# Kernel tuning notes

Hardware: AMD Instinct MI355X
Metric: run time of the kernel (lower is better)

Reference implementation:

```python
import jax, jax.numpy as jnp
import numpy as np

N = 8192
FIN = 128
FOUT = 64
NEG_BIG = -9e15


def setup_inputs() -> dict:
    key = jax.random.key(0)
    k1, k2, k3, k4 = jax.random.split(key, 4)
    x = jax.random.normal(k1, (N, FIN), dtype=jnp.float32)
    adj = jax.random.randint(k2, (N, N), 0, 2, dtype=jnp.int32)
    stdv_w = 1.0 / np.sqrt(FOUT)
    W = jax.random.uniform(k3, (FIN, FOUT), dtype=jnp.float32, minval=-stdv_w, maxval=stdv_w)
    # weight2: stdv = 1/sqrt(1) = 1
    a = jax.random.uniform(k4, (2 * FOUT, 1), dtype=jnp.float32, minval=-1.0, maxval=1.0)
    return {"x": x, "adj": adj, "W": W, "a": a}


def reference(x, adj, W, a):
    # h = x W  -> [N, Fout]
    h = x @ W
    # e_ij = relu(a^T [h_i || h_j]) decomposed exactly: a1.h_i + a2.h_j
    a1 = a[:FOUT, 0]  # [Fout]
    a2 = a[FOUT:, 0]  # [Fout]
    s1 = h @ a1  # [N]
    s2 = h @ a2  # [N]
    e = jax.nn.relu(s1[:, None] + s2[None, :])  # [N, N]
    att_logits = jnp.where(adj > 0, e, jnp.float32(NEG_BIG))
    attention = jax.nn.softmax(att_logits, axis=-1)  # [N, N]
    # dropout omitted (eval mode / p applied only in training)
    out = attention @ h  # [N, Fout]
    return out[None]  # [1, N, Fout] matching batch_size=1 reshape
```

## Files before the change

### kernel.cpp

```cpp
#include <hip/hip_runtime.h>
#include <cstdint>
#include <cstddef>

#define NN 8192
#define FIN 128
#define FOUT 64
#define BM 32
#define BN 64
#define JSPLIT 8
#define JCH (NN / JSPLIT)
#define NCHUNK (JCH / BN)
#define LDP 72

typedef __bf16 bf16x8 __attribute__((ext_vector_type(8)));
typedef unsigned short u16x8 __attribute__((ext_vector_type(8)));
typedef float f32x4 __attribute__((ext_vector_type(4)));

__device__ __forceinline__ unsigned short f2bf(float f) {
    unsigned u = __float_as_uint(f);
    u += 0x7FFFu + ((u >> 16) & 1u);
    return (unsigned short)(u >> 16);
}
__device__ __forceinline__ float bf2f(unsigned short b) {
    return __uint_as_float(((unsigned)b) << 16);
}

__global__ __launch_bounds__(256) void gat_prep(
    const float* __restrict__ x, const float* __restrict__ W,
    const float* __restrict__ a, float* __restrict__ s1,
    float* __restrict__ s2, unsigned short* __restrict__ Ht,
    unsigned int* __restrict__ s2max_enc)
{
    __shared__ __align__(16) float Wt[FOUT][FIN + 4];
    __shared__ float wa1[FIN], wa2[FIN];
    __shared__ float ash[2 * FOUT];
    __shared__ float s2sh[BM];

    const int tid = threadIdx.x;
    const int i0 = blockIdx.x * BM;

    for (int it = 0; it < 32; ++it) {
        int idx = it * 256 + tid;
        int k = idx >> 6, t = idx & 63;
        Wt[t][k] = W[idx];
    }
    if (tid < 2 * FOUT) ash[tid] = a[tid];
    __syncthreads();

    if (tid < FIN) {
        int k = tid;
        float acc = 0.f;
        #pragma unroll 8
        for (int t = 0; t < FOUT; ++t) acc = fmaf(Wt[t][k], ash[t], acc);
        wa1[k] = acc;
    } else {
        int k = tid - FIN;
        float acc = 0.f;
        #pragma unroll 8
        for (int t = 0; t < FOUT; ++t) acc = fmaf(Wt[t][k], ash[FOUT + t], acc);
        wa2[k] = acc;
    }
    __syncthreads();

    {
        int r = tid >> 3;
        int seg = tid & 7;
        const float* xp = x + (size_t)(i0 + r) * FIN + seg * 16;
        float d1 = 0.f, d2 = 0.f;
        #pragma unroll
        for (int m = 0; m < 16; ++m) {
            float xv = xp[m];
            d1 = fmaf(xv, wa1[seg * 16 + m], d1);
            d2 = fmaf(xv, wa2[seg * 16 + m], d2);
        }
        #pragma unroll
        for (int mk = 1; mk < 8; mk <<= 1) {
            d1 += __shfl_xor(d1, mk);
            d2 += __shfl_xor(d2, mk);
        }
        if (seg == 0) {
            s1[i0 + r] = d1;
            s2[i0 + r] = d2;
            s2sh[r] = d2;
        }
    }

    {
        const int lane = tid & 63;
        const int wv = tid >> 6;
        const int ih = wv & 1, nh = wv >> 1;
        const int m = lane & 15, quad = lane >> 4;
        f32x4 hacc0 = {0.f, 0.f, 0.f, 0.f};
        f32x4 hacc1 = {0.f, 0.f, 0.f, 0.f};
        const float* xrow = x + (size_t)(i0 + ih * 16 + m) * FIN + quad * 8;
        #pragma unroll
        for (int ks = 0; ks < 4; ++ks) {
            const float* xp = xrow + ks * 32;
            u16x8 ua;
            #pragma unroll
            for (int jj = 0; jj < 8; ++jj) ua[jj] = f2bf(xp[jj]);
            bf16x8 af = __builtin_bit_cast(bf16x8, ua);
            {
                const float* wp = &Wt[nh * 32 + m][ks * 32 + quad * 8];
                u16x8 ub;
                #pragma unroll
                for (int jj = 0; jj < 8; ++jj) ub[jj] = f2bf(wp[jj]);
                bf16x8 bfr = __builtin_bit_cast(bf16x8, ub);
                hacc0 = __builtin_amdgcn_mfma_f32_16x16x32_bf16(af, bfr, hacc0, 0, 0, 0);
            }
            {
                const float* wp = &Wt[nh * 32 + 16 + m][ks * 32 + quad * 8];
                u16x8 ub;
                #pragma unroll
                for (int jj = 0; jj < 8; ++jj) ub[jj] = f2bf(wp[jj]);
                bf16x8 bfr = __builtin_bit_cast(bf16x8, ub);
                hacc1 = __builtin_amdgcn_mfma_f32_16x16x32_bf16(af, bfr, hacc1, 0, 0, 0);
            }
        }
        #pragma unroll
        for (int reg = 0; reg < 4; ++reg) {
            int irow = i0 + ih * 16 + quad * 4 + reg;
            int t0 = nh * 32 + m;
            Ht[(size_t)t0 * NN + irow] = f2bf(hacc0[reg]);
            Ht[(size_t)(t0 + 16) * NN + irow] = f2bf(hacc1[reg]);
        }
    }
    __syncthreads();
    if (tid == 0) {
        float mx = s2sh[0];
        #pragma unroll
        for (int r = 1; r < BM; ++r) mx = fmaxf(mx, s2sh[r]);
        unsigned ub = __float_as_uint(mx);
        unsigned enc = (ub & 0x80000000u) ? ~ub : (ub | 0x80000000u);
        atomicMax(s2max_enc, enc);
    }
}

__global__ __launch_bounds__(256, 6) void gat_attn(
    const int* __restrict__ adj, const float* __restrict__ s1,
    const float* __restrict__ s2, const unsigned short* __restrict__ Ht,
    const unsigned int* __restrict__ s2max_enc,
    float* __restrict__ pacc, float* __restrict__ pl)
{
    __shared__ __align__(16) unsigned short p_lds[2][BM][LDP];
    __shared__ __align__(16) float s2sh[JCH];
    __shared__ float s1v[BM], Mv[BM];

    const int tid = threadIdx.x;
    const int bx = blockIdx.x;
    const int r = bx >> 3;
    const int js = bx & 7;
    const int i0 = r * BM;
    const int j0 = js * JCH;

    const int li = tid >> 4;
    const int jg = (tid & 15) * 4;

    const int* adjp0 = adj + (size_t)(i0 + li) * NN + j0 + jg;
    const int* adjp1 = adjp0 + 16 * NN;

    int4 ca0 = *(const int4*)adjp0;
    int4 ca1 = *(const int4*)adjp1;

    const int lane = tid & 63;
    const int wv = tid >> 6;
    const int ih = wv & 1, nh = wv >> 1;
    const int cm = lane & 15, quad = lane >> 4;

    const unsigned short* htb0 = Ht + (size_t)(nh * 32 + cm) * NN + j0 + quad * 8;
    const unsigned short* htb1 = htb0 + (size_t)16 * NN;

    {
        int idx = tid * 4;
        *(float4*)&s2sh[idx] = *(const float4*)(s2 + j0 + idx);
        unsigned u = *s2max_enc;
        float S2MAX = (u & 0x80000000u) ? __uint_as_float(u ^ 0x80000000u)
                                        : __uint_as_float(~u);
        if (tid < BM) {
            float s = s1[i0 + tid];
            s1v[tid] = s;
            Mv[tid] = fmaxf(0.f, s + S2MAX);
        }
    }
    __syncthreads();

    f32x4 acc0 = {0.f, 0.f, 0.f, 0.f};
    f32x4 acc1 = {0.f, 0.f, 0.f, 0.f};
    float psA = 0.f, psB = 0.f;

    const float s1a = s1v[li], Ma = Mv[li];
    const float s1b = s1v[li + 16], Mb = Mv[li + 16];

    for (int c = 0; c < NCHUNK; ++c) {
        const int buf = c & 1;

        bf16x8 b00 = *(const bf16x8*)(htb0 + c * BN);
        bf16x8 b01 = *(const bf16x8*)(htb1 + c * BN);
        bf16x8 b10 = *(const bf16x8*)(htb0 + c * BN + 32);
        bf16x8 b11 = *(const bf16x8*)(htb1 + c * BN + 32);

        const int cn = (c + 1 < NCHUNK) ? (c + 1) : c;
        int4 na0 = *(const int4*)(adjp0 + cn * BN);
        int4 na1 = *(const int4*)(adjp1 + cn * BN);

        {
            const int* av0 = (const int*)&ca0;
            const int* av1 = (const int*)&ca1;
            const float* s2v = &s2sh[c * BN + jg];
            unsigned short qa[4], qb[4];
            #pragma unroll
            for (int jj = 0; jj < 4; ++jj) {
                float s2x = s2v[jj];
                float eA = fmaxf(s1a + s2x, 0.f);
                float pA = (av0[jj] > 0) ? __expf(eA - Ma) : 0.f;
                qa[jj] = f2bf(pA);
                psA += bf2f(qa[jj]);
                float eB = fmaxf(s1b + s2x, 0.f);
                float pB = (av1[jj] > 0) ? __expf(eB - Mb) : 0.f;
                qb[jj] = f2bf(pB);
                psB += bf2f(qb[jj]);
            }
            *(ushort4*)&p_lds[buf][li][jg]      = make_ushort4(qa[0], qa[1], qa[2], qa[3]);
            *(ushort4*)&p_lds[buf][li + 16][jg] = make_ushort4(qb[0], qb[1], qb[2], qb[3]);
        }

        __syncthreads();

        {
            bf16x8 af0 = *(const bf16x8*)&p_lds[buf][ih * 16 + cm][quad * 8];
            bf16x8 af1 = *(const bf16x8*)&p_lds[buf][ih * 16 + cm][32 + quad * 8];
            acc0 = __builtin_amdgcn_mfma_f32_16x16x32_bf16(af0, b00, acc0, 0, 0, 0);
            acc1 = __builtin_amdgcn_mfma_f32_16x16x32_bf16(af0, b01, acc1, 0, 0, 0);
            acc0 = __builtin_amdgcn_mfma_f32_16x16x32_bf16(af1, b10, acc0, 0, 0, 0);
            acc1 = __builtin_amdgcn_mfma_f32_16x16x32_bf16(af1, b11, acc1, 0, 0, 0);
        }

        ca0 = na0; ca1 = na1;
    }

    #pragma unroll
    for (int mk = 1; mk < 16; mk <<= 1) {
        psA += __shfl_xor(psA, mk);
        psB += __shfl_xor(psB, mk);
    }
    if ((tid & 15) == 0) {
        pl[(size_t)js * NN + i0 + li]      = psA;
        pl[(size_t)js * NN + i0 + li + 16] = psB;
    }

    #pragma unroll
    for (int reg = 0; reg < 4; ++reg) {
        int irow = i0 + ih * 16 + quad * 4 + reg;
        int n0 = nh * 32 + cm;
        pacc[((size_t)js * NN + irow) * FOUT + n0]      = acc0[reg];
        pacc[((size_t)js * NN + irow) * FOUT + n0 + 16] = acc1[reg];
    }
}

__global__ __launch_bounds__(256) void gat_combine(
    const float* __restrict__ pacc, const float* __restrict__ pl,
    float* __restrict__ out)
{
    int idx = blockIdx.x * 256 + threadIdx.x;
    int i = idx >> 6;
    float s = 0.f, l = 0.f;
    #pragma unroll
    for (int js = 0; js < JSPLIT; ++js) {
        s += pacc[(size_t)js * NN * FOUT + idx];
        l += pl[(size_t)js * NN + i];
    }
    out[idx] = s / l;
}

extern "C" void kernel_launch(void* const* d_in, const int* in_sizes, int n_in,
                              void* d_out, int out_size, void* d_ws, size_t ws_size,
                              hipStream_t stream) {
    const float* x   = (const float*)d_in[0];
    const int*   adj = (const int*)d_in[1];
    const float* W   = (const float*)d_in[2];
    const float* a   = (const float*)d_in[3];
    float* out = (float*)d_out;

    char* ws = (char*)d_ws;
    float* s1             = (float*)(ws);
    float* s2             = (float*)(ws + 32768);
    unsigned int* s2enc   = (unsigned int*)(ws + 65536);
    unsigned short* Ht    = (unsigned short*)(ws + 66560);
    float* pacc           = (float*)(ws + 66560 + 1048576);
    float* pl             = (float*)(ws + 66560 + 1048576 + 16777216);

    hipMemsetAsync(s2enc, 0, 4, stream);
    gat_prep<<<NN / BM, 256, 0, stream>>>(x, W, a, s1, s2, Ht, s2enc);
    gat_attn<<<(NN / BM) * JSPLIT, 256, 0, stream>>>(adj, s1, s2, Ht, s2enc, pacc, pl);
    gat_combine<<<NN * FOUT / 256, 256, 0, stream>>>(pacc, pl, out);
}
```

Measured before the change: 401.0 us.

## Compute P directly in MFMA A-operand registers, drop LDS staging and barriers

Each lane now builds its own attention-probability fragment in the layout the bf16 MFMA A operand expects. This removes the shared-memory P buffer and the per-chunk __syncthreads. Each wave now owns 16 rows and all 64 output columns (four accumulators), so the block tile grows to 64 rows and the grid halves. The intent is to remove LDS traffic and barrier stalls in this adj-bandwidth-bound loop. The cost is more Ht loads per wave, higher register pressure, and lower occupancy (launch bound 4).

```diff
diff --git a/kernel.cpp b/kernel.cpp
--- a/kernel.cpp
+++ b/kernel.cpp
@@ -6,11 +6,10 @@
 #define FIN 128
 #define FOUT 64
 #define BM 32
-#define BN 64
+#define AM 64
 #define JSPLIT 8
 #define JCH (NN / JSPLIT)
-#define NCHUNK (JCH / BN)
-#define LDP 72
+#define NCHUNK (JCH / 64)
 
 typedef __bf16 bf16x8 __attribute__((ext_vector_type(8)));
 typedef unsigned short u16x8 __attribute__((ext_vector_type(8)));
@@ -136,124 +135,118 @@
     }
 }
 
-__global__ __launch_bounds__(256, 6) void gat_attn(
+__device__ __forceinline__ void make_p(const int4 A, const int4 B,
+                                       const float* __restrict__ s2p,
+                                       float s1r, float M,
+                                       u16x8& ua, float& ps)
+{
+    const int av[8] = {A.x, A.y, A.z, A.w, B.x, B.y, B.z, B.w};
+    #pragma unroll
+    for (int jj = 0; jj < 8; ++jj) {
+        float e = fmaxf(s1r + s2p[jj], 0.f);
+        float pv = (av[jj] > 0) ? __expf(e - M) : 0.f;
+        unsigned short qv = f2bf(pv);
+        ua[jj] = qv;
+        ps += bf2f(qv);
+    }
+}
+
+__global__ __launch_bounds__(256, 4) void gat_attn(
     const int* __restrict__ adj, const float* __restrict__ s1,
     const float* __restrict__ s2, const unsigned short* __restrict__ Ht,
     const unsigned int* __restrict__ s2max_enc,
     float* __restrict__ pacc, float* __restrict__ pl)
 {
-    __shared__ __align__(16) unsigned short p_lds[2][BM][LDP];
     __shared__ __align__(16) float s2sh[JCH];
-    __shared__ float s1v[BM], Mv[BM];
 
     const int tid = threadIdx.x;
     const int bx = blockIdx.x;
     const int r = bx >> 3;
     const int js = bx & 7;
-    const int i0 = r * BM;
+    const int i0 = r * AM;
     const int j0 = js * JCH;
 
-    const int li = tid >> 4;
-    const int jg = (tid & 15) * 4;
-
-    const int* adjp0 = adj + (size_t)(i0 + li) * NN + j0 + jg;
-    const int* adjp1 = adjp0 + 16 * NN;
-
-    int4 ca0 = *(const int4*)adjp0;
-    int4 ca1 = *(const int4*)adjp1;
-
     const int lane = tid & 63;
-    const int wv = tid >> 6;
-    const int ih = wv & 1, nh = wv >> 1;
-    const int cm = lane & 15, quad = lane >> 4;
-
-    const unsigned short* htb0 = Ht + (size_t)(nh * 32 + cm) * NN + j0 + quad * 8;
-    const unsigned short* htb1 = htb0 + (size_t)16 * NN;
+    const int w = tid >> 6;
+    const int m = lane & 15;
+    const int q = lane >> 4;
+
+    const int irow = i0 + w * 16 + m;
 
     {
         int idx = tid * 4;
         *(float4*)&s2sh[idx] = *(const float4*)(s2 + j0 + idx);
-        unsigned u = *s2max_enc;
-        float S2MAX = (u & 0x80000000u) ? __uint_as_float(u ^ 0x80000000u)
-                                        : __uint_as_float(~u);
-        if (tid < BM) {
-            float s = s1[i0 + tid];
-            s1v[tid] = s;
-            Mv[tid] = fmaxf(0.f, s + S2MAX);
-        }
-    }
-    __syncthreads();
+    }
+    unsigned u = *s2max_enc;
+    const float S2MAX = (u & 0x80000000u) ? __uint_as_float(u ^ 0x80000000u)
+                                          : __uint_as_float(~u);
+    const float s1r = s1[irow];
+    const float M = fmaxf(0.f, s1r + S2MAX);
+    __syncthreads();
+
+    const int* adjr = adj + (size_t)irow * NN + j0 + q * 8;
+    const unsigned short* htb = Ht + (size_t)m * NN + j0 + q * 8;
 
     f32x4 acc0 = {0.f, 0.f, 0.f, 0.f};
     f32x4 acc1 = {0.f, 0.f, 0.f, 0.f};
-    float psA = 0.f, psB = 0.f;
-
-    const float s1a = s1v[li], Ma = Mv[li];
-    const float s1b = s1v[li + 16], Mb = Mv[li + 16];
+    f32x4 acc2 = {0.f, 0.f, 0.f, 0.f};
+    f32x4 acc3 = {0.f, 0.f, 0.f, 0.f};
+    float ps = 0.f;
+
+    int4 c0a = *(const int4*)(adjr);
+    int4 c0b = *(const int4*)(adjr + 4);
+    int4 c1a = *(const int4*)(adjr + 32);
+    int4 c1b = *(const int4*)(adjr + 36);
 
     for (int c = 0; c < NCHUNK; ++c) {
-        const int buf = c & 1;
-
-        bf16x8 b00 = *(const bf16x8*)(htb0 + c * BN);
-        bf16x8 b01 = *(const bf16x8*)(htb1 + c * BN);
-        bf16x8 b10 = *(const bf16x8*)(htb0 + c * BN + 32);
-        bf16x8 b11 = *(const bf16x8*)(htb1 + c * BN + 32);
-
-        const int cn = (c + 1 < NCHUNK) ? (c + 1) : c;
-        int4 na0 = *(const int4*)(adjp0 + cn * BN);
-        int4 na1 = *(const int4*)(adjp1 + cn * BN);
-
-        {
-            const int* av0 = (const int*)&ca0;
-            const int* av1 = (const int*)&ca1;
-            const float* s2v = &s2sh[c * BN + jg];
-            unsigned short qa[4], qb[4];
-            #pragma unroll
-            for (int jj = 0; jj < 4; ++jj) {
-                float s2x = s2v[jj];
-                float eA = fmaxf(s1a + s2x, 0.f);
-                float pA = (av0[jj] > 0) ? __expf(eA - Ma) : 0.f;
-                qa[jj] = f2bf(pA);
-                psA += bf2f(qa[jj]);
-                float eB = fmaxf(s1b + s2x, 0.f);
-                float pB = (av1[jj] > 0) ? __expf(eB - Mb) : 0.f;
-                qb[jj] = f2bf(pB);
-                psB += bf2f(qb[jj]);
-            }
-            *(ushort4*)&p_lds[buf][li][jg]      = make_ushort4(qa[0], qa[1], qa[2], qa[3]);
-            *(ushort4*)&p_lds[buf][li + 16][jg] = make_ushort4(qb[0], qb[1], qb[2], qb[3]);
-        }
-
-        __syncthreads();
-
-        {
-            bf16x8 af0 = *(const bf16x8*)&p_lds[buf][ih * 16 + cm][quad * 8];
-            bf16x8 af1 = *(const bf16x8*)&p_lds[buf][ih * 16 + cm][32 + quad * 8];
-            acc0 = __builtin_amdgcn_mfma_f32_16x16x32_bf16(af0, b00, acc0, 0, 0, 0);
-            acc1 = __builtin_amdgcn_mfma_f32_16x16x32_bf16(af0, b01, acc1, 0, 0, 0);
-            acc0 = __builtin_amdgcn_mfma_f32_16x16x32_bf16(af1, b10, acc0, 0, 0, 0);
-            acc1 = __builtin_amdgcn_mfma_f32_16x16x32_bf16(af1, b11, acc1, 0, 0, 0);
-        }
-
-        ca0 = na0; ca1 = na1;
-    }
-
-    #pragma unroll
-    for (int mk = 1; mk < 16; mk <<= 1) {
-        psA += __shfl_xor(psA, mk);
-        psB += __shfl_xor(psB, mk);
-    }
-    if ((tid & 15) == 0) {
-        pl[(size_t)js * NN + i0 + li]      = psA;
-        pl[(size_t)js * NN + i0 + li + 16] = psB;
-    }
-
+        const int cn = (c + 1 < NCHUNK) ? c + 1 : c;
+        const int* an = adjr + cn * 64;
+        int4 n0a = *(const int4*)(an);
+        int4 n0b = *(const int4*)(an + 4);
+        int4 n1a = *(const int4*)(an + 32);
+        int4 n1b = *(const int4*)(an + 36);
+
+        const unsigned short* hb = htb + c * 64;
+        bf16x8 b00 = *(const bf16x8*)(hb);
+        bf16x8 b01 = *(const bf16x8*)(hb + 32);
+        bf16x8 b10 = *(const bf16x8*)(hb + (size_t)16 * NN);
+        bf16x8 b11 = *(const bf16x8*)(hb + (size_t)16 * NN + 32);
+        bf16x8 b20 = *(const bf16x8*)(hb + (size_t)32 * NN);
+        bf16x8 b21 = *(const bf16x8*)(hb + (size_t)32 * NN + 32);
+        bf16x8 b30 = *(const bf16x8*)(hb + (size_t)48 * NN);
+        bf16x8 b31 = *(const bf16x8*)(hb + (size_t)48 * NN + 32);
+
+        const float* s2p = &s2sh[c * 64 + q * 8];
+        u16x8 ua0, ua1;
+        make_p(c0a, c0b, s2p,      s1r, M, ua0, ps);
+        make_p(c1a, c1b, s2p + 32, s1r, M, ua1, ps);
+        bf16x8 af0 = __builtin_bit_cast(bf16x8, ua0);
+        bf16x8 af1 = __builtin_bit_cast(bf16x8, ua1);
+
+        acc0 = __builtin_amdgcn_mfma_f32_16x16x32_bf16(af0, b00, acc0, 0, 0, 0);
+        acc1 = __builtin_amdgcn_mfma_f32_16x16x32_bf16(af0, b10, acc1, 0, 0, 0);
+        acc2 = __builtin_amdgcn_mfma_f32_16x16x32_bf16(af0, b20, acc2, 0, 0, 0);
+        acc3 = __builtin_amdgcn_mfma_f32_16x16x32_bf16(af0, b30, acc3, 0, 0, 0);
+        acc0 = __builtin_amdgcn_mfma_f32_16x16x32_bf16(af1, b01, acc0, 0, 0, 0);
+        acc1 = __builtin_amdgcn_mfma_f32_16x16x32_bf16(af1, b11, acc1, 0, 0, 0);
+        acc2 = __builtin_amdgcn_mfma_f32_16x16x32_bf16(af1, b21, acc2, 0, 0, 0);
+        acc3 = __builtin_amdgcn_mfma_f32_16x16x32_bf16(af1, b31, acc3, 0, 0, 0);
+
+        c0a = n0a; c0b = n0b; c1a = n1a; c1b = n1b;
+    }
+
+    ps += __shfl_xor(ps, 16);
+    ps += __shfl_xor(ps, 32);
+    if (q == 0) pl[(size_t)js * NN + irow] = ps;
+
+    const int orow = i0 + w * 16 + q * 4;
+    float* pb = pacc + ((size_t)js * NN + orow) * FOUT + m;
     #pragma unroll
     for (int reg = 0; reg < 4; ++reg) {
-        int irow = i0 + ih * 16 + quad * 4 + reg;
-        int n0 = nh * 32 + cm;
-        pacc[((size_t)js * NN + irow) * FOUT + n0]      = acc0[reg];
-        pacc[((size_t)js * NN + irow) * FOUT + n0 + 16] = acc1[reg];
+        pb[(size_t)reg * FOUT]      = acc0[reg];
+        pb[(size_t)reg * FOUT + 16] = acc1[reg];
+        pb[(size_t)reg * FOUT + 32] = acc2[reg];
+        pb[(size_t)reg * FOUT + 48] = acc3[reg];
     }
 }
 
@@ -291,6 +284,6 @@
 
     hipMemsetAsync(s2enc, 0, 4, stream);
     gat_prep<<<NN / BM, 256, 0, stream>>>(x, W, a, s1, s2, Ht, s2enc);
-    gat_attn<<<(NN / BM) * JSPLIT, 256, 0, stream>>>(adj, s1, s2, Ht, s2enc, pacc, pl);
+    gat_attn<<<(NN / AM) * JSPLIT, 256, 0, stream>>>(adj, s1, s2, Ht, s2enc, pacc, pl);
     gat_combine<<<NN * FOUT / 256, 256, 0, stream>>>(pacc, pl, out);
 }
```

Result: no change. 408.6 us (+1.9%).
